# Performance work log

Measured on AMD Instinct MI355X. Metric: run time of the kernel, lower is better.

The kernel has to match this reference:

```python
import jax, jax.numpy as jnp
import numpy as np

HEAD_DIM = 64
HIDDEN_SIZE = 3072
NUM_HEADS = 48
B, TXT, VID = 1, 256, 1792
N = TXT + VID


def _layernorm(x, g, b, eps=1e-5):
    mu = jnp.mean(x, axis=-1, keepdims=True)
    xc = x - mu
    var = jnp.mean(xc * xc, axis=-1, keepdims=True)
    return xc * jax.lax.rsqrt(var + eps) * g + b


def _apply_rope1(x, freqs):
    # x: [B, L, H, D]; freqs: [1, 1, Lf, D//2, 2, 2]
    Bx, L, H, D = x.shape
    x_ = x.reshape(Bx, L, H, D // 2, 1, 2)
    # faithful to torch: if dim-2 sizes mismatch (H vs Lf), slice freqs to H
    if x_.shape[2] != 1 and freqs.shape[2] != 1 and x_.shape[2] != freqs.shape[2]:
        freqs = freqs[:, :, : x_.shape[2]]
    out = freqs[..., 0] * x_[..., 0] + freqs[..., 1] * x_[..., 1]
    return out.reshape(Bx, L, H, D).astype(x.dtype)


def setup_inputs() -> dict:
    key = jax.random.key(0)
    ks = jax.random.split(key, 16)
    s = 1.0 / np.sqrt(HIDDEN_SIZE)
    d = dict(
        combined=jax.random.normal(ks[0], (B, N, HIDDEN_SIZE), jnp.float32),
        freqs=jax.random.normal(ks[1], (1, 1, VID, HEAD_DIM // 2, 2, 2), jnp.float32),
        Wq=jax.random.normal(ks[2], (HIDDEN_SIZE, HIDDEN_SIZE), jnp.float32) * s,
        bq=jnp.zeros((HIDDEN_SIZE,), jnp.float32),
        Wk=jax.random.normal(ks[3], (HIDDEN_SIZE, HIDDEN_SIZE), jnp.float32) * s,
        bk=jnp.zeros((HIDDEN_SIZE,), jnp.float32),
        Wv=jax.random.normal(ks[4], (HIDDEN_SIZE, HIDDEN_SIZE), jnp.float32) * s,
        bv=jnp.zeros((HIDDEN_SIZE,), jnp.float32),
        Wo=jax.random.normal(ks[5], (HIDDEN_SIZE, HIDDEN_SIZE), jnp.float32) * s,
        bo=jnp.zeros((HIDDEN_SIZE,), jnp.float32),
        gq=jnp.ones((HEAD_DIM,), jnp.float32),
        bgq=jnp.zeros((HEAD_DIM,), jnp.float32),
        gk=jnp.ones((HEAD_DIM,), jnp.float32),
        bgk=jnp.zeros((HEAD_DIM,), jnp.float32),
        txt_len=TXT,
    )
    return d


def reference(combined, freqs, Wq, bq, Wk, bk, Wv, bv, Wo, bo, gq, bgq, gk, bgk, txt_len):
    Bx, Nx, _ = combined.shape
    Q = (combined @ Wq.T + bq).reshape(Bx, Nx, NUM_HEADS, HEAD_DIM)
    K = (combined @ Wk.T + bk).reshape(Bx, Nx, NUM_HEADS, HEAD_DIM)
    V = (combined @ Wv.T + bv).reshape(Bx, Nx, NUM_HEADS, HEAD_DIM)
    Q = _layernorm(Q, gq, bgq)
    K = _layernorm(K, gk, bgk)
    if freqs is not None and Nx - txt_len > 0:
        Q_vid = _apply_rope1(Q[:, txt_len:], freqs)
        K_vid = _apply_rope1(K[:, txt_len:], freqs)
        Q = jnp.concatenate([Q[:, :txt_len], Q_vid], axis=1)
        K = jnp.concatenate([K[:, :txt_len], K_vid], axis=1)
    # SDPA in fp32: [B, H, N, D]
    q = Q.transpose(0, 2, 1, 3).astype(jnp.float32)
    k = K.transpose(0, 2, 1, 3).astype(jnp.float32)
    v = V.transpose(0, 2, 1, 3).astype(jnp.float32)
    scale = 1.0 / np.sqrt(HEAD_DIM)
    scores = jnp.einsum('bhqd,bhkd->bhqk', q, k) * scale
    probs = jax.nn.softmax(scores, axis=-1)
    attn = jnp.einsum('bhqk,bhkd->bhqd', probs, v).astype(combined.dtype)
    attn = attn.transpose(0, 2, 1, 3).reshape(Bx, Nx, HIDDEN_SIZE)
    out = attn @ Wo.T + bo
    return out[:, txt_len:], out[:, :txt_len]
```

## Files before the change

kernel.cpp:

```cpp
#include <hip/hip_runtime.h>
#include <hip/hip_bf16.h>

typedef __attribute__((ext_vector_type(8))) short bf16x8;
typedef __attribute__((ext_vector_type(4))) float f32x4;
typedef unsigned int __attribute__((address_space(1))) as1_uint;
typedef unsigned int __attribute__((address_space(3))) as3_uint;

#define TXT 256
#define VIDN 1792
#define SEQ 2048
#define HID 3072
#define NH 48
#define HD 64
#define QSCALE 0.18033688011112042f

__device__ __forceinline__ unsigned short f2bf(float f) {
  union { float f; unsigned int u; } x; x.f = f;
  unsigned int r = x.u + 0x7fffu + ((x.u >> 16) & 1u);
  return (unsigned short)(r >> 16);
}

__device__ __forceinline__ void gload16(const void* g, void* l) {
  __builtin_amdgcn_global_load_lds((const as1_uint*)g, (as3_uint*)l, 16, 0, 0);
}

__global__ __launch_bounds__(256) void cvt_kernel(const float* __restrict__ s,
                                                  unsigned short* __restrict__ d, int n) {
  int i = (blockIdx.x * 256 + threadIdx.x) * 4;
  if (i >= n) return;
  float4 v = *(const float4*)(s + i);
  ushort4 o;
  o.x = f2bf(v.x); o.y = f2bf(v.y); o.z = f2bf(v.z); o.w = f2bf(v.w);
  *(ushort4*)(d + i) = o;
}

template<int MODE>
__global__ __launch_bounds__(256) void gemm_bt(
    const unsigned short* __restrict__ A,
    const unsigned short* __restrict__ Bt,
    int K, int ntn,
    float* __restrict__ Cq, unsigned short* __restrict__ VtOut, const float* __restrict__ bv,
    float* __restrict__ Cout, const float* __restrict__ bo)
{
  __shared__ unsigned short la[128 * 32];
  __shared__ unsigned short lb[128 * 32];
  const int tid = threadIdx.x;
  const int mt = blockIdx.x / ntn, nt = blockIdx.x % ntn;
  const int m0 = mt * 128, n0 = nt * 128;
  const int w = tid >> 6, lane = tid & 63, lr = lane & 15, lg = lane >> 4;
  const int wm = (w >> 1) * 64, wn = (w & 1) * 64;
  f32x4 acc[4][4] = {};
  for (int k0 = 0; k0 < K; k0 += 32) {
#pragma unroll
    for (int c = 0; c < 2; ++c) {
      int off = (c * 256 + tid) * 16;
      int row = off >> 6, cb = off & 63;
      gload16(A + (size_t)(m0 + row) * K + k0 + (cb >> 1), (char*)la + off);
      gload16(Bt + (size_t)(n0 + row) * K + k0 + (cb >> 1), (char*)lb + off);
    }
    __syncthreads();
    bf16x8 af[4], bfr[4];
#pragma unroll
    for (int f = 0; f < 4; ++f) {
      af[f]  = *(const bf16x8*)&la[(wm + f * 16 + lr) * 32 + lg * 8];
      bfr[f] = *(const bf16x8*)&lb[(wn + f * 16 + lr) * 32 + lg * 8];
    }
#pragma unroll
    for (int mf = 0; mf < 4; ++mf)
#pragma unroll
      for (int nf = 0; nf < 4; ++nf)
        acc[mf][nf] = __builtin_amdgcn_mfma_f32_16x16x32_bf16(af[mf], bfr[nf], acc[mf][nf], 0, 0, 0);
    __syncthreads();
  }

  if (MODE == 0) {
    if (n0 < 6144) {
#pragma unroll
      for (int mf = 0; mf < 4; ++mf)
#pragma unroll
        for (int nf = 0; nf < 4; ++nf) {
          int row = m0 + wm + mf * 16 + lg * 4;
          int col = n0 + wn + nf * 16 + lr;
#pragma unroll
          for (int j = 0; j < 4; ++j)
            Cq[(size_t)(row + j) * 6144 + col] = acc[mf][nf][j];
        }
    } else {
#pragma unroll
      for (int mf = 0; mf < 4; ++mf)
#pragma unroll
        for (int nf = 0; nf < 4; ++nf) {
          int srow = m0 + wm + mf * 16 + lg * 4;
          int n2 = n0 - 6144 + wn + nf * 16 + lr;
          float b = bv[n2];
          ushort4 pk;
          pk.x = f2bf(acc[mf][nf][0] + b);
          pk.y = f2bf(acc[mf][nf][1] + b);
          pk.z = f2bf(acc[mf][nf][2] + b);
          pk.w = f2bf(acc[mf][nf][3] + b);
          *(ushort4*)(VtOut + (size_t)n2 * SEQ + srow) = pk;
        }
    }
  } else {
#pragma unroll
    for (int mf = 0; mf < 4; ++mf)
#pragma unroll
      for (int nf = 0; nf < 4; ++nf) {
        int row = m0 + wm + mf * 16 + lg * 4;
        int col = n0 + wn + nf * 16 + lr;
        float b = bo[col];
#pragma unroll
        for (int j = 0; j < 4; ++j) {
          int s = row + j;
          int orow = (s >= TXT) ? (s - TXT) : (VIDN + s);
          Cout[(size_t)orow * HID + col] = acc[mf][nf][j] + b;
        }
      }
  }
}

__global__ __launch_bounds__(256) void ln_rope_kernel(
    const float* __restrict__ QK,
    const float* __restrict__ bq, const float* __restrict__ bk,
    const float* __restrict__ gq, const float* __restrict__ bgq,
    const float* __restrict__ gk, const float* __restrict__ bgk,
    const float* __restrict__ freqs,
    unsigned short* __restrict__ Qh, unsigned short* __restrict__ Kh)
{
  int wid = blockIdx.x * 4 + (threadIdx.x >> 6);
  int lane = threadIdx.x & 63;
  int s = wid / 96;
  int rem = wid - s * 96;
  int h = rem >> 1, qk = rem & 1;
  int col = h * 64 + lane;
  float x = QK[(size_t)s * 6144 + qk * 3072 + col] + (qk ? bk[col] : bq[col]);
  float m = x;
#pragma unroll
  for (int msk = 1; msk < 64; msk <<= 1) m += __shfl_xor(m, msk);
  float mu = m * (1.0f / 64.0f);
  float xc = x - mu;
  float v = xc * xc;
#pragma unroll
  for (int msk = 1; msk < 64; msk <<= 1) v += __shfl_xor(v, msk);
  float rstd = rsqrtf(v * (1.0f / 64.0f) + 1e-5f);
  float y = xc * rstd * (qk ? gk[lane] : gq[lane]) + (qk ? bgk[lane] : bgq[lane]);
  if (s >= TXT) {
    float p = __shfl_xor(y, 1);
    float xe = (lane & 1) ? p : y;
    float xo = (lane & 1) ? y : p;
    int base = h * 128 + (lane >> 1) * 4 + (lane & 1) * 2;
    y = freqs[base] * xe + freqs[base + 1] * xo;
  }
  if (!qk) y *= QSCALE;
  (qk ? Kh : Qh)[((size_t)h * SEQ + s) * 64 + lane] = f2bf(y);
}

__global__ __launch_bounds__(256) void fattn_kernel(
    const unsigned short* __restrict__ Qh, const unsigned short* __restrict__ Kh,
    const unsigned short* __restrict__ Vt, unsigned short* __restrict__ ctx)
{
  __shared__ unsigned short kt[2][64][32];
  __shared__ unsigned short vt[2][64][32];
  __shared__ unsigned short pl[4][16][72];
  const int h = blockIdx.x >> 5;
  const int q0 = (blockIdx.x & 31) * 64;
  const int tid = threadIdx.x, w = tid >> 6, lane = tid & 63, lr = lane & 15, lg = lane >> 4;

  bf16x8 qf0, qf1;
  {
    const unsigned short* qp = Qh + ((size_t)h * SEQ + q0 + w * 16 + lr) * 64 + lg * 8;
    qf0 = *(const bf16x8*)qp;
    qf1 = *(const bf16x8*)(qp + 32);
  }
  f32x4 oacc[4] = {};
  float mrun = -1e30f, lrun = 0.f;

  for (int kv0 = 0; kv0 < SEQ; kv0 += 64) {
    __syncthreads();
#pragma unroll
    for (int c = 0; c < 2; ++c) {
      int off = (c * 256 + tid) * 16;
      int half = off >> 12;
      int rem = off & 4095;
      int row = rem >> 6, cb = rem & 63;
      gload16(Kh + ((size_t)h * SEQ + kv0 + row) * 64 + half * 32 + (cb >> 1), (char*)kt + off);
      gload16(Vt + ((size_t)(h * 64 + row)) * SEQ + kv0 + half * 32 + (cb >> 1), (char*)vt + off);
    }
    __syncthreads();

    f32x4 sacc[4] = {};
    __builtin_amdgcn_s_setprio(1);
#pragma unroll
    for (int nf = 0; nf < 4; ++nf) {
      bf16x8 a0 = *(const bf16x8*)&kt[0][nf * 16 + lr][lg * 8];
      bf16x8 a1 = *(const bf16x8*)&kt[1][nf * 16 + lr][lg * 8];
      sacc[nf] = __builtin_amdgcn_mfma_f32_16x16x32_bf16(a0, qf0, sacc[nf], 0, 0, 0);
      sacc[nf] = __builtin_amdgcn_mfma_f32_16x16x32_bf16(a1, qf1, sacc[nf], 0, 0, 0);
    }
    __builtin_amdgcn_s_setprio(0);

    float mx;
    {
      float t0 = fmaxf(fmaxf(sacc[0][0], sacc[0][1]), fmaxf(sacc[0][2], sacc[0][3]));
      float t1 = fmaxf(fmaxf(sacc[1][0], sacc[1][1]), fmaxf(sacc[1][2], sacc[1][3]));
      float t2 = fmaxf(fmaxf(sacc[2][0], sacc[2][1]), fmaxf(sacc[2][2], sacc[2][3]));
      float t3 = fmaxf(fmaxf(sacc[3][0], sacc[3][1]), fmaxf(sacc[3][2], sacc[3][3]));
      mx = fmaxf(fmaxf(t0, t1), fmaxf(t2, t3));
    }
    mx = fmaxf(mx, __shfl_xor(mx, 16));
    mx = fmaxf(mx, __shfl_xor(mx, 32));

    if (!__all(mx <= mrun + 8.0f)) {
      float mn = fmaxf(mrun, mx);
      float corr = exp2f(mrun - mn);
      lrun *= corr;
      mrun = mn;
      float c0 = __shfl(corr, lg * 4 + 0);
      float c1 = __shfl(corr, lg * 4 + 1);
      float c2 = __shfl(corr, lg * 4 + 2);
      float c3 = __shfl(corr, lg * 4 + 3);
#pragma unroll
      for (int df = 0; df < 4; ++df) {
        oacc[df][0] *= c0; oacc[df][1] *= c1;
        oacc[df][2] *= c2; oacc[df][3] *= c3;
      }
    }

    float pr[4][4];
#pragma unroll
    for (int nf = 0; nf < 4; ++nf)
#pragma unroll
      for (int r = 0; r < 4; ++r)
        pr[nf][r] = exp2f(sacc[nf][r] - mrun);
    float rs;
    {
      float s0 = (pr[0][0] + pr[0][1]) + (pr[0][2] + pr[0][3]);
      float s1 = (pr[1][0] + pr[1][1]) + (pr[1][2] + pr[1][3]);
      float s2 = (pr[2][0] + pr[2][1]) + (pr[2][2] + pr[2][3]);
      float s3 = (pr[3][0] + pr[3][1]) + (pr[3][2] + pr[3][3]);
      rs = (s0 + s1) + (s2 + s3);
    }
    rs += __shfl_xor(rs, 16);
    rs += __shfl_xor(rs, 32);
    lrun += rs;

#pragma unroll
    for (int nf = 0; nf < 4; ++nf) {
      union { __hip_bfloat162 h; unsigned int u; } c0, c1;
      c0.h = __float22bfloat162_rn(make_float2(pr[nf][0], pr[nf][1]));
      c1.h = __float22bfloat162_rn(make_float2(pr[nf][2], pr[nf][3]));
      uint2 pw; pw.x = c0.u; pw.y = c1.u;
      *(uint2*)&pl[w][lr][nf * 16 + lg * 4] = pw;
    }

    bf16x8 pa0 = *(const bf16x8*)&pl[w][lr][lg * 8];
    bf16x8 pa1 = *(const bf16x8*)&pl[w][lr][32 + lg * 8];
    __builtin_amdgcn_s_setprio(1);
#pragma unroll
    for (int df = 0; df < 4; ++df) {
      bf16x8 v0 = *(const bf16x8*)&vt[0][df * 16 + lr][lg * 8];
      bf16x8 v1 = *(const bf16x8*)&vt[1][df * 16 + lr][lg * 8];
      oacc[df] = __builtin_amdgcn_mfma_f32_16x16x32_bf16(pa0, v0, oacc[df], 0, 0, 0);
      oacc[df] = __builtin_amdgcn_mfma_f32_16x16x32_bf16(pa1, v1, oacc[df], 0, 0, 0);
    }
    __builtin_amdgcn_s_setprio(0);
  }

  float linv = 1.0f / lrun;
  float i0 = __shfl(linv, lg * 4 + 0);
  float i1 = __shfl(linv, lg * 4 + 1);
  float i2 = __shfl(linv, lg * 4 + 2);
  float i3 = __shfl(linv, lg * 4 + 3);
#pragma unroll
  for (int df = 0; df < 4; ++df) {
    int s = q0 + w * 16 + lg * 4;
    int dcol = h * 64 + df * 16 + lr;
    ctx[(size_t)(s + 0) * HID + dcol] = f2bf(oacc[df][0] * i0);
    ctx[(size_t)(s + 1) * HID + dcol] = f2bf(oacc[df][1] * i1);
    ctx[(size_t)(s + 2) * HID + dcol] = f2bf(oacc[df][2] * i2);
    ctx[(size_t)(s + 3) * HID + dcol] = f2bf(oacc[df][3] * i3);
  }
}

extern "C" void kernel_launch(void* const* d_in, const int* in_sizes, int n_in,
                              void* d_out, int out_size, void* d_ws, size_t ws_size,
                              hipStream_t stream) {
  const float* combined = (const float*)d_in[0];
  const float* freqs    = (const float*)d_in[1];
  const float* Wq  = (const float*)d_in[2];
  const float* bq  = (const float*)d_in[3];
  const float* Wk  = (const float*)d_in[4];
  const float* bk  = (const float*)d_in[5];
  const float* Wv  = (const float*)d_in[6];
  const float* bv  = (const float*)d_in[7];
  const float* Wo  = (const float*)d_in[8];
  const float* bo  = (const float*)d_in[9];
  const float* gq  = (const float*)d_in[10];
  const float* bgq = (const float*)d_in[11];
  const float* gk  = (const float*)d_in[12];
  const float* bgk = (const float*)d_in[13];
  float* out = (float*)d_out;

  char* ws = (char*)d_ws;
  unsigned short* Abf  = (unsigned short*)ws; ws += (size_t)SEQ * HID * 2;
  unsigned short* Wqkv = (unsigned short*)ws; ws += (size_t)3 * HID * HID * 2;
  float*          QK   = (float*)ws;          ws += (size_t)SEQ * 6144 * 4;
  unsigned short* Qh   = (unsigned short*)ws; ws += (size_t)NH * SEQ * HD * 2;
  unsigned short* Kh   = (unsigned short*)ws; ws += (size_t)NH * SEQ * HD * 2;
  unsigned short* Vt   = (unsigned short*)ws; ws += (size_t)NH * HD * SEQ * 2;
  unsigned short* Wob  = (unsigned short*)QK;
  unsigned short* ctx  = Abf;

  cvt_kernel<<<(SEQ * HID) / 1024, 256, 0, stream>>>(combined, Abf, SEQ * HID);
  cvt_kernel<<<(HID * HID) / 1024, 256, 0, stream>>>(Wq, Wqkv, HID * HID);
  cvt_kernel<<<(HID * HID) / 1024, 256, 0, stream>>>(Wk, Wqkv + (size_t)HID * HID, HID * HID);
  cvt_kernel<<<(HID * HID) / 1024, 256, 0, stream>>>(Wv, Wqkv + (size_t)2 * HID * HID, HID * HID);

  gemm_bt<0><<<16 * 72, 256, 0, stream>>>(Abf, Wqkv, HID, 72, QK, Vt, bv, nullptr, nullptr);

  ln_rope_kernel<<<(SEQ * NH * 2) / 4, 256, 0, stream>>>(QK, bq, bk, gq, bgq, gk, bgk, freqs, Qh, Kh);

  cvt_kernel<<<(HID * HID) / 1024, 256, 0, stream>>>(Wo, Wob, HID * HID);

  fattn_kernel<<<NH * 32, 256, 0, stream>>>(Qh, Kh, Vt, ctx);

  gemm_bt<1><<<16 * 24, 256, 0, stream>>>(ctx, Wob, HID, 24, nullptr, nullptr, nullptr, out, bo);
}
```

Before: 469.4 us.

## Fuse QK layernorm and RoPE into QKV GEMM epilogue, merge weight conversions

Moves the per-head layernorm, bias add, RoPE and Q scaling into the QKV GEMM epilogue, using 16-lane shuffles over the accumulator layout. This removes the fp32 QK intermediate buffer and the separate ln_rope kernel, saving a large global write and re-read. It also merges the three Wq/Wk/Wv conversions into one launch and adds an XCD-aware block index swizzle for the GEMMs. In exchange, the epilogue does more register work and scattered 2-byte stores.

```diff
diff --git a/kernel.cpp b/kernel.cpp
--- a/kernel.cpp
+++ b/kernel.cpp
@@ -34,18 +34,40 @@
   *(ushort4*)(d + i) = o;
 }
 
+__global__ __launch_bounds__(256) void cvt3_kernel(const float* __restrict__ a,
+                                                   const float* __restrict__ b,
+                                                   const float* __restrict__ c,
+                                                   unsigned short* __restrict__ d) {
+  const int per = (HID * HID) / 1024;
+  int bid = blockIdx.x;
+  int m = bid / per, r = bid - m * per;
+  const float* s = (m == 0) ? a : (m == 1) ? b : c;
+  int i = (r * 256 + threadIdx.x) * 4;
+  float4 v = *(const float4*)(s + i);
+  ushort4 o;
+  o.x = f2bf(v.x); o.y = f2bf(v.y); o.z = f2bf(v.z); o.w = f2bf(v.w);
+  *(ushort4*)(d + (size_t)m * HID * HID + i) = o;
+}
+
 template<int MODE>
 __global__ __launch_bounds__(256) void gemm_bt(
     const unsigned short* __restrict__ A,
     const unsigned short* __restrict__ Bt,
     int K, int ntn,
-    float* __restrict__ Cq, unsigned short* __restrict__ VtOut, const float* __restrict__ bv,
+    unsigned short* __restrict__ Qh, unsigned short* __restrict__ Kh,
+    unsigned short* __restrict__ Vt, const float* __restrict__ bv,
+    const float* __restrict__ bq, const float* __restrict__ bk,
+    const float* __restrict__ gq, const float* __restrict__ bgq,
+    const float* __restrict__ gk, const float* __restrict__ bgk,
+    const float* __restrict__ freqs,
     float* __restrict__ Cout, const float* __restrict__ bo)
 {
   __shared__ unsigned short la[128 * 32];
   __shared__ unsigned short lb[128 * 32];
   const int tid = threadIdx.x;
-  const int mt = blockIdx.x / ntn, nt = blockIdx.x % ntn;
+  const int cpx = gridDim.x >> 3;
+  const int swz = (blockIdx.x & 7) * cpx + (blockIdx.x >> 3);
+  const int mt = swz / ntn, nt = swz % ntn;
   const int m0 = mt * 128, n0 = nt * 128;
   const int w = tid >> 6, lane = tid & 63, lr = lane & 15, lg = lane >> 4;
   const int wm = (w >> 1) * 64, wn = (w & 1) * 64;
@@ -75,16 +97,60 @@
 
   if (MODE == 0) {
     if (n0 < 6144) {
-#pragma unroll
-      for (int mf = 0; mf < 4; ++mf)
-#pragma unroll
-        for (int nf = 0; nf < 4; ++nf) {
-          int row = m0 + wm + mf * 16 + lg * 4;
-          int col = n0 + wn + nf * 16 + lr;
-#pragma unroll
-          for (int j = 0; j < 4; ++j)
-            Cq[(size_t)(row + j) * 6144 + col] = acc[mf][nf][j];
+      const bool isQ = (n0 < 3072);
+      const int h = ((n0 - (isQ ? 0 : 3072)) + wn) >> 6;
+      const float* bias = isQ ? bq : bk;
+      const float* gg   = isQ ? gq : gk;
+      const float* bg   = isQ ? bgq : bgk;
+      unsigned short* dst = isQ ? Qh : Kh;
+      float gv[4], bgv[4], bi[4], fe[4], fo[4];
+#pragma unroll
+      for (int nf = 0; nf < 4; ++nf) {
+        int c = nf * 16 + lr;
+        gv[nf]  = gg[c];
+        bgv[nf] = bg[c];
+        bi[nf]  = bias[h * 64 + c];
+        int base = h * 128 + (c >> 1) * 4 + (c & 1) * 2;
+        fe[nf] = freqs[base];
+        fo[nf] = freqs[base + 1];
+      }
+#pragma unroll
+      for (int mf = 0; mf < 4; ++mf) {
+        const bool rope = (m0 + wm + mf * 16) >= TXT;
+#pragma unroll
+        for (int j = 0; j < 4; ++j) {
+          int row = m0 + wm + mf * 16 + lg * 4 + j;
+          float x[4], sum = 0.f;
+#pragma unroll
+          for (int nf = 0; nf < 4; ++nf) { x[nf] = acc[mf][nf][j] + bi[nf]; sum += x[nf]; }
+          sum += __shfl_xor(sum, 1); sum += __shfl_xor(sum, 2);
+          sum += __shfl_xor(sum, 4); sum += __shfl_xor(sum, 8);
+          float mu = sum * (1.0f / 64.0f);
+          float var = 0.f;
+#pragma unroll
+          for (int nf = 0; nf < 4; ++nf) { x[nf] -= mu; var += x[nf] * x[nf]; }
+          var += __shfl_xor(var, 1); var += __shfl_xor(var, 2);
+          var += __shfl_xor(var, 4); var += __shfl_xor(var, 8);
+          float rstd = rsqrtf(var * (1.0f / 64.0f) + 1e-5f);
+          float y[4];
+#pragma unroll
+          for (int nf = 0; nf < 4; ++nf) y[nf] = x[nf] * rstd * gv[nf] + bgv[nf];
+          if (rope) {
+#pragma unroll
+            for (int nf = 0; nf < 4; ++nf) {
+              float p = __shfl_xor(y[nf], 1);
+              float xe = (lr & 1) ? p : y[nf];
+              float xo = (lr & 1) ? y[nf] : p;
+              y[nf] = fe[nf] * xe + fo[nf] * xo;
+            }
+          }
+#pragma unroll
+          for (int nf = 0; nf < 4; ++nf) {
+            float v = isQ ? y[nf] * QSCALE : y[nf];
+            dst[((size_t)h * SEQ + row) * 64 + nf * 16 + lr] = f2bf(v);
+          }
         }
+      }
     } else {
 #pragma unroll
       for (int mf = 0; mf < 4; ++mf)
@@ -98,7 +164,7 @@
           pk.y = f2bf(acc[mf][nf][1] + b);
           pk.z = f2bf(acc[mf][nf][2] + b);
           pk.w = f2bf(acc[mf][nf][3] + b);
-          *(ushort4*)(VtOut + (size_t)n2 * SEQ + srow) = pk;
+          *(ushort4*)(Vt + (size_t)n2 * SEQ + srow) = pk;
         }
     }
   } else {
@@ -117,42 +183,6 @@
         }
       }
   }
-}
-
-__global__ __launch_bounds__(256) void ln_rope_kernel(
-    const float* __restrict__ QK,
-    const float* __restrict__ bq, const float* __restrict__ bk,
-    const float* __restrict__ gq, const float* __restrict__ bgq,
-    const float* __restrict__ gk, const float* __restrict__ bgk,
-    const float* __restrict__ freqs,
-    unsigned short* __restrict__ Qh, unsigned short* __restrict__ Kh)
-{
-  int wid = blockIdx.x * 4 + (threadIdx.x >> 6);
-  int lane = threadIdx.x & 63;
-  int s = wid / 96;
-  int rem = wid - s * 96;
-  int h = rem >> 1, qk = rem & 1;
-  int col = h * 64 + lane;
-  float x = QK[(size_t)s * 6144 + qk * 3072 + col] + (qk ? bk[col] : bq[col]);
-  float m = x;
-#pragma unroll
-  for (int msk = 1; msk < 64; msk <<= 1) m += __shfl_xor(m, msk);
-  float mu = m * (1.0f / 64.0f);
-  float xc = x - mu;
-  float v = xc * xc;
-#pragma unroll
-  for (int msk = 1; msk < 64; msk <<= 1) v += __shfl_xor(v, msk);
-  float rstd = rsqrtf(v * (1.0f / 64.0f) + 1e-5f);
-  float y = xc * rstd * (qk ? gk[lane] : gq[lane]) + (qk ? bgk[lane] : bgq[lane]);
-  if (s >= TXT) {
-    float p = __shfl_xor(y, 1);
-    float xe = (lane & 1) ? p : y;
-    float xo = (lane & 1) ? y : p;
-    int base = h * 128 + (lane >> 1) * 4 + (lane & 1) * 2;
-    y = freqs[base] * xe + freqs[base + 1] * xo;
-  }
-  if (!qk) y *= QSCALE;
-  (qk ? Kh : Qh)[((size_t)h * SEQ + s) * 64 + lane] = f2bf(y);
 }
 
 __global__ __launch_bounds__(256) void fattn_kernel(
@@ -304,25 +334,27 @@
   char* ws = (char*)d_ws;
   unsigned short* Abf  = (unsigned short*)ws; ws += (size_t)SEQ * HID * 2;
   unsigned short* Wqkv = (unsigned short*)ws; ws += (size_t)3 * HID * HID * 2;
-  float*          QK   = (float*)ws;          ws += (size_t)SEQ * 6144 * 4;
+  unsigned short* Wob  = (unsigned short*)ws; ws += (size_t)HID * HID * 2;
   unsigned short* Qh   = (unsigned short*)ws; ws += (size_t)NH * SEQ * HD * 2;
   unsigned short* Kh   = (unsigned short*)ws; ws += (size_t)NH * SEQ * HD * 2;
   unsigned short* Vt   = (unsigned short*)ws; ws += (size_t)NH * HD * SEQ * 2;
-  unsigned short* Wob  = (unsigned short*)QK;
   unsigned short* ctx  = Abf;
 
   cvt_kernel<<<(SEQ * HID) / 1024, 256, 0, stream>>>(combined, Abf, SEQ * HID);
-  cvt_kernel<<<(HID * HID) / 1024, 256, 0, stream>>>(Wq, Wqkv, HID * HID);
-  cvt_kernel<<<(HID * HID) / 1024, 256, 0, stream>>>(Wk, Wqkv + (size_t)HID * HID, HID * HID);
-  cvt_kernel<<<(HID * HID) / 1024, 256, 0, stream>>>(Wv, Wqkv + (size_t)2 * HID * HID, HID * HID);
-
-  gemm_bt<0><<<16 * 72, 256, 0, stream>>>(Abf, Wqkv, HID, 72, QK, Vt, bv, nullptr, nullptr);
-
-  ln_rope_kernel<<<(SEQ * NH * 2) / 4, 256, 0, stream>>>(QK, bq, bk, gq, bgq, gk, bgk, freqs, Qh, Kh);
+  cvt3_kernel<<<3 * (HID * HID) / 1024, 256, 0, stream>>>(Wq, Wk, Wv, Wqkv);
+
+  gemm_bt<0><<<16 * 72, 256, 0, stream>>>(Abf, Wqkv, HID, 72,
+                                          Qh, Kh, Vt, bv,
+                                          bq, bk, gq, bgq, gk, bgk, freqs,
+                                          nullptr, nullptr);
 
   cvt_kernel<<<(HID * HID) / 1024, 256, 0, stream>>>(Wo, Wob, HID * HID);
 
   fattn_kernel<<<NH * 32, 256, 0, stream>>>(Qh, Kh, Vt, ctx);
 
-  gemm_bt<1><<<16 * 24, 256, 0, stream>>>(ctx, Wob, HID, 24, nullptr, nullptr, nullptr, out, bo);
-}
+  gemm_bt<1><<<16 * 24, 256, 0, stream>>>(ctx, Wob, HID, 24,
+                                          nullptr, nullptr, nullptr, nullptr,
+                                          nullptr, nullptr, nullptr, nullptr,
+                                          nullptr, nullptr, nullptr,
+                                          out, bo);
+}
```

New measurement: 478.8 us. 2.0% more time.
